# Kernel optimization log

Hardware: AMD Instinct MI355X
Metric: run time of the kernel (lower is better)

The kernel has to match this reference:

```python
import jax, jax.numpy as jnp
import numpy as np

N_NODES = 100000
N_EDGES = 1600000
IN_FEATS = 128
HEADS = 4
OUT_FEATS = 16
NEG_SLOPE = 0.2  # DGL GATConv default negative_slope


def setup_inputs() -> dict:
    key = jax.random.key(0)
    ks = jax.random.split(key, 7)
    feats = jax.random.normal(ks[0], (N_NODES, IN_FEATS), dtype=jnp.float32)
    W = jax.random.normal(ks[1], (HEADS * OUT_FEATS, IN_FEATS), dtype=jnp.float32) * 0.05
    attn_l = jax.random.normal(ks[2], (HEADS, OUT_FEATS), dtype=jnp.float32) * 0.1
    attn_r = jax.random.normal(ks[3], (HEADS, OUT_FEATS), dtype=jnp.float32) * 0.1
    bias = jax.random.normal(ks[4], (HEADS * OUT_FEATS,), dtype=jnp.float32) * 0.01
    src = jax.random.randint(ks[5], (N_EDGES,), 0, N_NODES, dtype=jnp.int64 if jax.config.jax_enable_x64 else jnp.int32)
    dst = jax.random.randint(ks[6], (N_EDGES,), 0, N_NODES, dtype=jnp.int64 if jax.config.jax_enable_x64 else jnp.int32)
    return {"feats": feats, "W": W, "attn_l": attn_l, "attn_r": attn_r,
            "bias": bias, "src": src, "dst": dst}


def reference(feats, W, attn_l, attn_r, bias, src, dst):
    """GATConv forward on a homogeneous graph built from concatenated edge lists.

    feats: [N, in_feats]; W: [H*F, in_feats]; attn_l/attn_r: [H, F]; bias: [H*F]
    src/dst: [E] edge endpoint indices. Returns [N, H, F] (DGL GATConv output).
    """
    N = feats.shape[0]
    H, F = attn_l.shape
    # Linear projection, per-head split: z [N, H, F]
    z = (feats @ W.T).reshape(N, H, F)
    # Per-node attention logits: el/er [N, H]
    el = jnp.einsum('nhf,hf->nh', z, attn_l)
    er = jnp.einsum('nhf,hf->nh', z, attn_r)
    # Per-edge unnormalized attention: e [E, H]
    e = jax.nn.leaky_relu(el[src] + er[dst], negative_slope=NEG_SLOPE)
    # Edge softmax over incoming edges of each destination node
    m = jax.ops.segment_max(e, dst, num_segments=N)           # [N, H]
    m = jnp.where(jnp.isfinite(m), m, jnp.zeros_like(m))      # guard empty segments
    ex = jnp.exp(e - m[dst])                                  # [E, H]
    denom = jax.ops.segment_sum(ex, dst, num_segments=N)      # [N, H]
    alpha = ex / denom[dst]                                   # [E, H]
    # Weighted message aggregation: scatter-add z[src] * alpha into dst
    msg = z[src] * alpha[:, :, None]                          # [E, H, F]
    out = jax.ops.segment_sum(msg, dst, num_segments=N)       # [N, H, F]
    return out + bias.reshape(1, H, F)
```

## Files before the change

kernel.cpp:

```cpp
#include <hip/hip_runtime.h>

#define N_NODES 100000
#define N_EDGES 1600000
#define IN_F    128
#define HEADS   4
#define OUT_F   16
#define HF      64
#define NEG_SLOPE 0.2f
#define NB_MFMA 1563

#define BUCK    112
#define NBUCK   893
#define BSTRIDE 2048
#define BSC_CHUNK 6144
#define NB_BSC  261
#define BUCK3   56
#define K3_BLOCKS 1786

typedef __attribute__((ext_vector_type(8))) short short8;
typedef __attribute__((ext_vector_type(4))) float f32x4;

__device__ __forceinline__ short f2bf(float f) {
    union { float f; unsigned u; } v; v.f = f;
    return (short)((v.u + 0x7FFFu + ((v.u >> 16) & 1u)) >> 16);
}

__global__ __launch_bounds__(256) void k_prep(const float* __restrict__ W,
                                              const float* __restrict__ attn_l,
                                              const float* __restrict__ attn_r,
                                              unsigned short* __restrict__ Wfrag,
                                              int* __restrict__ gcur) {
    __shared__ float Bext[16 * IN_F];
    int t = threadIdx.x;
    for (int i = t; i < NBUCK; i += 256) gcur[i] = 0;
    for (int o = t; o < 16 * IN_F; o += 256) {
        int c = o >> 7, k = o & 127;
        float v = 0.f;
        if (c < 8) {
            int hh = c & 3;
            const float* at = (c < 4) ? attn_l : attn_r;
            #pragma unroll
            for (int f = 0; f < 16; ++f)
                v += W[(size_t)(hh * 16 + f) * IN_F + k] * at[hh * 16 + f];
        }
        Bext[o] = v;
    }
    __syncthreads();
    for (int idx = t; idx < 20 * 64 * 8; idx += 256) {
        int j = idx & 7;
        int lane = (idx >> 3) & 63;
        int g = idx >> 9;
        int ct = g >> 2, kf = g & 3;
        int n = lane & 15, qq = lane >> 4;
        int k = kf * 32 + qq * 8 + j;
        float val = (ct < 4) ? W[(size_t)(ct * 16 + n) * IN_F + k]
                             : Bext[n * IN_F + k];
        Wfrag[idx] = (unsigned short)f2bf(val);
    }
}

__global__ __launch_bounds__(256) void k1_mfma(const float* __restrict__ feats,
                                               const unsigned short* __restrict__ Wfrag,
                                               unsigned short* __restrict__ zb,
                                               float* __restrict__ el,
                                               float* __restrict__ er) {
    const int t = threadIdx.x;
    const int grp = t >> 6;
    const int l = t & 63;
    const int q = l >> 4, n = l & 15;

    short8 bfrag[5][4];
    #pragma unroll
    for (int ct = 0; ct < 5; ++ct)
        #pragma unroll
        for (int kf = 0; kf < 4; ++kf)
            bfrag[ct][kf] = *(const short8*)(Wfrag + (size_t)((ct * 4 + kf) * 64 + l) * 8);

    int anode = blockIdx.x * 64 + grp * 16 + n;
    int aclamp = anode < N_NODES ? anode : 0;
    const float* arow = feats + (size_t)aclamp * IN_F + q * 8;

    f32x4 acc[5];
    #pragma unroll
    for (int ct = 0; ct < 5; ++ct) acc[ct] = (f32x4){0.f, 0.f, 0.f, 0.f};

    #pragma unroll
    for (int kf = 0; kf < 4; ++kf) {
        float4 x = *(const float4*)(arow + kf * 32);
        float4 y = *(const float4*)(arow + kf * 32 + 4);
        short8 a;
        a[0] = f2bf(x.x); a[1] = f2bf(x.y); a[2] = f2bf(x.z); a[3] = f2bf(x.w);
        a[4] = f2bf(y.x); a[5] = f2bf(y.y); a[6] = f2bf(y.z); a[7] = f2bf(y.w);
        #pragma unroll
        for (int ct = 0; ct < 5; ++ct)
            acc[ct] = __builtin_amdgcn_mfma_f32_16x16x32_bf16(a, bfrag[ct][kf], acc[ct], 0, 0, 0);
    }

    #pragma unroll
    for (int reg = 0; reg < 4; ++reg) {
        int onode = blockIdx.x * 64 + grp * 16 + q * 4 + reg;
        if (onode >= N_NODES) continue;
        #pragma unroll
        for (int ct = 0; ct < 4; ++ct)
            zb[(size_t)onode * HF + ct * 16 + n] = (unsigned short)f2bf(acc[ct][reg]);
        float v4 = acc[4][reg];
        if (n < 4)       el[onode * HEADS + n] = v4;
        else if (n < 8)  er[onode * HEADS + (n - 4)] = v4;
    }
}

__global__ __launch_bounds__(1024) void k_bsc(const int* __restrict__ src,
                                              const int* __restrict__ dst,
                                              int* __restrict__ gcur,
                                              unsigned* __restrict__ bin) {
    __shared__ int h[NBUCK], cur[NBUCK];
    const int t = threadIdx.x;
    if (t < NBUCK) { h[t] = 0; }
    __syncthreads();
    const int start = blockIdx.x * BSC_CHUNK;
    int end = start + BSC_CHUNK;
    if (end > N_EDGES) end = N_EDGES;

    int myd[6];
    #pragma unroll
    for (int k = 0; k < 6; ++k) {
        int i = start + t + k * 1024;
        myd[k] = (i < end) ? dst[i] : -1;
        if (myd[k] >= 0) atomicAdd(&h[(unsigned)myd[k] / BUCK], 1);
    }
    __syncthreads();
    if (t < NBUCK) cur[t] = h[t] ? atomicAdd(&gcur[t], h[t]) : 0;
    __syncthreads();
    #pragma unroll
    for (int k = 0; k < 6; ++k) {
        int i = start + t + k * 1024;
        if (i < end) {
            unsigned d = (unsigned)myd[k];
            unsigned b = d / BUCK;
            unsigned dl = d - b * BUCK;
            int pos = atomicAdd(&cur[b], 1);
            if (pos < BSTRIDE)
                bin[(size_t)b * BSTRIDE + pos] = (unsigned)src[i] | (dl << 17);
        }
    }
}

__global__ __launch_bounds__(256) void k3_sort(const unsigned* __restrict__ bin,
                                               const int* __restrict__ gcur,
                                               const float* __restrict__ el,
                                               const float* __restrict__ er,
                                               const unsigned short* __restrict__ zb,
                                               const float* __restrict__ bias,
                                               float* __restrict__ out) {
    __shared__ unsigned raw[BSTRIDE];
    __shared__ unsigned sorted[BSTRIDE];
    __shared__ int hist[BUCK3];
    __shared__ int noff[BUCK3 + 1];
    __shared__ int cur[BUCK3];
    __shared__ int s[64];
    __shared__ float er_s[BUCK3 * HEADS];

    const int t = threadIdx.x;
    const int B2 = blockIdx.x >> 1;
    const int half = blockIdx.x & 1;
    const int dlo = half * BUCK3;
    const int nodebase = B2 * BUCK + dlo;
    const unsigned* mybin = bin + (size_t)B2 * BSTRIDE;
    int cnt = gcur[B2];
    if (cnt > BSTRIDE) cnt = BSTRIDE;

    if (t < BUCK3) hist[t] = 0;
    if (t < BUCK3 * HEADS) {
        int g = nodebase * HEADS + t;
        er_s[t] = (g < N_NODES * HEADS) ? er[g] : 0.f;
    }
    for (int i = t; i < cnt; i += 256) raw[i] = mybin[i];
    __syncthreads();

    for (int i = t; i < cnt; i += 256) {
        int d2 = (int)(raw[i] >> 17) - dlo;
        if ((unsigned)d2 < BUCK3) atomicAdd(&hist[d2], 1);
    }
    __syncthreads();

    if (t < 64) s[t] = (t < BUCK3) ? hist[t] : 0;
    __syncthreads();
    for (int o = 1; o < 64; o <<= 1) {
        int x = (t < 64 && t >= o) ? s[t - o] : 0;
        __syncthreads();
        if (t < 64) s[t] += x;
        __syncthreads();
    }
    if (t < BUCK3) {
        int excl = s[t] - hist[t];
        noff[t] = excl;
        cur[t] = excl;
    }
    if (t == 0) noff[BUCK3] = s[BUCK3 - 1];
    __syncthreads();

    for (int i = t; i < cnt; i += 256) {
        unsigned p = raw[i];
        int d2 = (int)(p >> 17) - dlo;
        if ((unsigned)d2 < BUCK3) {
            int pos = atomicAdd(&cur[d2], 1);
            sorted[pos] = p & 0x1FFFF;
        }
    }
    __syncthreads();

    const int wave = t >> 6, lane = t & 63;
    const int j = lane >> 3;
    const int c = lane & 7;
    const int h = c >> 1;

    for (int nl = wave; nl < BUCK3; nl += 4) {
        int node = nodebase + nl;
        if (node >= N_NODES) break;
        const int nlo = noff[nl], nhi = noff[nl + 1];
        const float er_d = er_s[nl * HEADS + h];

        float4 A0 = make_float4(0.f, 0.f, 0.f, 0.f);
        float4 A1 = make_float4(0.f, 0.f, 0.f, 0.f);
        float den = 0.f;
        for (int i = nlo + j; i < nhi; i += 8) {
            int sN = sorted[i];
            float x = el[sN * HEADS + h] + er_d;
            x = x > 0.f ? x : NEG_SLOPE * x;
            float ex = __expf(x);
            den += ex;
            uint4 v = *(const uint4*)(zb + (size_t)sN * HF + c * 8);
            A0.x += ex * __uint_as_float(v.x << 16);
            A0.y += ex * __uint_as_float(v.x & 0xFFFF0000u);
            A0.z += ex * __uint_as_float(v.y << 16);
            A0.w += ex * __uint_as_float(v.y & 0xFFFF0000u);
            A1.x += ex * __uint_as_float(v.z << 16);
            A1.y += ex * __uint_as_float(v.z & 0xFFFF0000u);
            A1.z += ex * __uint_as_float(v.w << 16);
            A1.w += ex * __uint_as_float(v.w & 0xFFFF0000u);
        }
        #pragma unroll
        for (int m = 8; m <= 32; m <<= 1) {
            A0.x += __shfl_xor(A0.x, m); A0.y += __shfl_xor(A0.y, m);
            A0.z += __shfl_xor(A0.z, m); A0.w += __shfl_xor(A0.w, m);
            A1.x += __shfl_xor(A1.x, m); A1.y += __shfl_xor(A1.y, m);
            A1.z += __shfl_xor(A1.z, m); A1.w += __shfl_xor(A1.w, m);
            den  += __shfl_xor(den,  m);
        }
        if (j == 0) {
            float4 b0 = *(const float4*)(bias + c * 8);
            float4 b1 = *(const float4*)(bias + c * 8 + 4);
            if (den > 0.f) {
                float inv = 1.f / den;
                b0.x += A0.x * inv; b0.y += A0.y * inv;
                b0.z += A0.z * inv; b0.w += A0.w * inv;
                b1.x += A1.x * inv; b1.y += A1.y * inv;
                b1.z += A1.z * inv; b1.w += A1.w * inv;
            }
            *(float4*)(out + (size_t)node * HF + c * 8) = b0;
            *(float4*)(out + (size_t)node * HF + c * 8 + 4) = b1;
        }
    }
}

extern "C" void kernel_launch(void* const* d_in, const int* in_sizes, int n_in,
                              void* d_out, int out_size, void* d_ws, size_t ws_size,
                              hipStream_t stream) {
    const float* feats  = (const float*)d_in[0];
    const float* W      = (const float*)d_in[1];
    const float* attn_l = (const float*)d_in[2];
    const float* attn_r = (const float*)d_in[3];
    const float* bias   = (const float*)d_in[4];
    const int*   src    = (const int*)d_in[5];
    const int*   dst    = (const int*)d_in[6];
    float* out = (float*)d_out;

    char* ws = (char*)d_ws;
    unsigned short* zb = (unsigned short*)ws;  ws += (size_t)N_NODES * HF * 2;
    float* el    = (float*)ws;                 ws += N_NODES * HEADS * 4;
    float* er    = (float*)ws;                 ws += N_NODES * HEADS * 4;
    unsigned short* Wfrag = (unsigned short*)ws; ws += 20 * 64 * 8 * 2;
    int*   gcur  = (int*)ws;                   ws += 1024 * 4;
    unsigned* bin = (unsigned*)ws;             ws += (size_t)NBUCK * BSTRIDE * 4;

    k_prep  <<<1,         256,  0, stream>>>(W, attn_l, attn_r, Wfrag, gcur);
    k1_mfma <<<NB_MFMA,   256,  0, stream>>>(feats, Wfrag, zb, el, er);
    k_bsc   <<<NB_BSC,    1024, 0, stream>>>(src, dst, gcur, bin);
    k3_sort <<<K3_BLOCKS, 256,  0, stream>>>(bin, gcur, el, er, zb, bias, out);
}
```

Before: 189.5 us.

## Use coarser dst buckets with ballot compaction in sort-aggregate kernel

Replaces the 893 fine destination buckets with 224 coarse buckets of 448 nodes, so the binning pass runs fewer global atomics and writes less scattered output. Each k3 block now takes a 112-node sub-range, uses 512 threads, and compacts its matching edges from the coarse bin into shared memory with wave ballot and popcount before the histogram and sort. Each block now reads the whole coarse bin (about four times the data it needs), which trades extra read traffic for cheaper scattering. The MFMA kernel also switches to packed bf16 conversion intrinsics.

```diff
diff --git a/kernel.cpp b/kernel.cpp
--- a/kernel.cpp
+++ b/kernel.cpp
@@ -1,4 +1,5 @@
 #include <hip/hip_runtime.h>
+#include <hip/hip_bf16.h>
 
 #define N_NODES 100000
 #define N_EDGES 1600000
@@ -9,13 +10,15 @@
 #define NEG_SLOPE 0.2f
 #define NB_MFMA 1563
 
-#define BUCK    112
-#define NBUCK   893
-#define BSTRIDE 2048
+#define CBUCK   448
+#define NCB     224
+#define CSTRIDE 7936
 #define BSC_CHUNK 6144
 #define NB_BSC  261
-#define BUCK3   56
-#define K3_BLOCKS 1786
+
+#define SUB     112
+#define K3_BLOCKS 896
+#define RAWCAP  2304
 
 typedef __attribute__((ext_vector_type(8))) short short8;
 typedef __attribute__((ext_vector_type(4))) float f32x4;
@@ -23,6 +26,12 @@
 __device__ __forceinline__ short f2bf(float f) {
     union { float f; unsigned u; } v; v.f = f;
     return (short)((v.u + 0x7FFFu + ((v.u >> 16) & 1u)) >> 16);
+}
+
+__device__ __forceinline__ unsigned pkbf(float a, float b) {
+    __hip_bfloat162 t = __float22bfloat162_rn(make_float2(a, b));
+    unsigned r; __builtin_memcpy(&r, &t, sizeof(r));
+    return r;
 }
 
 __global__ __launch_bounds__(256) void k_prep(const float* __restrict__ W,
@@ -32,7 +41,7 @@
                                               int* __restrict__ gcur) {
     __shared__ float Bext[16 * IN_F];
     int t = threadIdx.x;
-    for (int i = t; i < NBUCK; i += 256) gcur[i] = 0;
+    for (int i = t; i < 1024; i += 256) gcur[i] = 0;
     for (int o = t; o < 16 * IN_F; o += 256) {
         int c = o >> 7, k = o & 127;
         float v = 0.f;
@@ -89,8 +98,11 @@
         float4 x = *(const float4*)(arow + kf * 32);
         float4 y = *(const float4*)(arow + kf * 32 + 4);
         short8 a;
-        a[0] = f2bf(x.x); a[1] = f2bf(x.y); a[2] = f2bf(x.z); a[3] = f2bf(x.w);
-        a[4] = f2bf(y.x); a[5] = f2bf(y.y); a[6] = f2bf(y.z); a[7] = f2bf(y.w);
+        unsigned* au = (unsigned*)&a;
+        au[0] = pkbf(x.x, x.y);
+        au[1] = pkbf(x.z, x.w);
+        au[2] = pkbf(y.x, y.y);
+        au[3] = pkbf(y.z, y.w);
         #pragma unroll
         for (int ct = 0; ct < 5; ++ct)
             acc[ct] = __builtin_amdgcn_mfma_f32_16x16x32_bf16(a, bfrag[ct][kf], acc[ct], 0, 0, 0);
@@ -113,9 +125,9 @@
                                               const int* __restrict__ dst,
                                               int* __restrict__ gcur,
                                               unsigned* __restrict__ bin) {
-    __shared__ int h[NBUCK], cur[NBUCK];
+    __shared__ int h[NCB], cur[NCB];
     const int t = threadIdx.x;
-    if (t < NBUCK) { h[t] = 0; }
+    if (t < NCB) h[t] = 0;
     __syncthreads();
     const int start = blockIdx.x * BSC_CHUNK;
     int end = start + BSC_CHUNK;
@@ -126,95 +138,109 @@
     for (int k = 0; k < 6; ++k) {
         int i = start + t + k * 1024;
         myd[k] = (i < end) ? dst[i] : -1;
-        if (myd[k] >= 0) atomicAdd(&h[(unsigned)myd[k] / BUCK], 1);
-    }
-    __syncthreads();
-    if (t < NBUCK) cur[t] = h[t] ? atomicAdd(&gcur[t], h[t]) : 0;
+        if (myd[k] >= 0) atomicAdd(&h[(unsigned)myd[k] / CBUCK], 1);
+    }
+    __syncthreads();
+    if (t < NCB) cur[t] = h[t] ? atomicAdd(&gcur[t], h[t]) : 0;
     __syncthreads();
     #pragma unroll
     for (int k = 0; k < 6; ++k) {
         int i = start + t + k * 1024;
         if (i < end) {
             unsigned d = (unsigned)myd[k];
-            unsigned b = d / BUCK;
-            unsigned dl = d - b * BUCK;
+            unsigned b = d / CBUCK;
+            unsigned dl = d - b * CBUCK;
             int pos = atomicAdd(&cur[b], 1);
-            if (pos < BSTRIDE)
-                bin[(size_t)b * BSTRIDE + pos] = (unsigned)src[i] | (dl << 17);
-        }
-    }
-}
-
-__global__ __launch_bounds__(256) void k3_sort(const unsigned* __restrict__ bin,
+            if (pos < CSTRIDE)
+                bin[(size_t)b * CSTRIDE + pos] = (unsigned)src[i] | (dl << 17);
+        }
+    }
+}
+
+__global__ __launch_bounds__(512) void k3_sort(const unsigned* __restrict__ bin,
                                                const int* __restrict__ gcur,
                                                const float* __restrict__ el,
                                                const float* __restrict__ er,
                                                const unsigned short* __restrict__ zb,
                                                const float* __restrict__ bias,
                                                float* __restrict__ out) {
-    __shared__ unsigned raw[BSTRIDE];
-    __shared__ unsigned sorted[BSTRIDE];
-    __shared__ int hist[BUCK3];
-    __shared__ int noff[BUCK3 + 1];
-    __shared__ int cur[BUCK3];
-    __shared__ int s[64];
-    __shared__ float er_s[BUCK3 * HEADS];
+    __shared__ unsigned raw[RAWCAP];
+    __shared__ unsigned sorted[RAWCAP];
+    __shared__ int hist[SUB];
+    __shared__ int noff[SUB + 1];
+    __shared__ int cur[SUB];
+    __shared__ int s[128];
+    __shared__ float er_s[SUB * HEADS];
+    __shared__ int rawcnt;
 
     const int t = threadIdx.x;
-    const int B2 = blockIdx.x >> 1;
-    const int half = blockIdx.x & 1;
-    const int dlo = half * BUCK3;
-    const int nodebase = B2 * BUCK + dlo;
-    const unsigned* mybin = bin + (size_t)B2 * BSTRIDE;
-    int cnt = gcur[B2];
-    if (cnt > BSTRIDE) cnt = BSTRIDE;
-
-    if (t < BUCK3) hist[t] = 0;
-    if (t < BUCK3 * HEADS) {
+    const int B = blockIdx.x >> 2;
+    const int sub = blockIdx.x & 3;
+    const int dlo = sub * SUB;
+    const int nodebase = B * CBUCK + dlo;
+    const unsigned* mybin = bin + (size_t)B * CSTRIDE;
+    int cnt = gcur[B];
+    if (cnt > CSTRIDE) cnt = CSTRIDE;
+
+    if (t < SUB) hist[t] = 0;
+    if (t == 0) rawcnt = 0;
+    if (t < SUB * HEADS) {
         int g = nodebase * HEADS + t;
         er_s[t] = (g < N_NODES * HEADS) ? er[g] : 0.f;
     }
-    for (int i = t; i < cnt; i += 256) raw[i] = mybin[i];
-    __syncthreads();
-
-    for (int i = t; i < cnt; i += 256) {
-        int d2 = (int)(raw[i] >> 17) - dlo;
-        if ((unsigned)d2 < BUCK3) atomicAdd(&hist[d2], 1);
-    }
-    __syncthreads();
-
-    if (t < 64) s[t] = (t < BUCK3) ? hist[t] : 0;
-    __syncthreads();
-    for (int o = 1; o < 64; o <<= 1) {
-        int x = (t < 64 && t >= o) ? s[t - o] : 0;
+    __syncthreads();
+
+    const int lane = t & 63;
+    for (int i0 = 0; i0 < cnt; i0 += 512) {
+        int e = i0 + t;
+        bool valid = e < cnt;
+        unsigned p = valid ? mybin[e] : 0u;
+        int d2 = (int)(p >> 17) - dlo;
+        bool match = valid && ((unsigned)d2 < (unsigned)SUB);
+        unsigned long long mask = __ballot(match);
+        int wbase = 0;
+        if (lane == 0) wbase = atomicAdd(&rawcnt, __popcll(mask));
+        wbase = __shfl(wbase, 0, 64);
+        int pos = wbase + __popcll(mask & ((1ull << lane) - 1ull));
+        if (match && pos < RAWCAP)
+            raw[pos] = (p & 0x1FFFFu) | ((unsigned)d2 << 17);
+    }
+    __syncthreads();
+    int rn = rawcnt < RAWCAP ? rawcnt : RAWCAP;
+
+    for (int i = t; i < rn; i += 512)
+        atomicAdd(&hist[raw[i] >> 17], 1);
+    __syncthreads();
+
+    if (t < 128) s[t] = (t < SUB) ? hist[t] : 0;
+    __syncthreads();
+    for (int o = 1; o < 128; o <<= 1) {
+        int x = (t < 128 && t >= o) ? s[t - o] : 0;
         __syncthreads();
-        if (t < 64) s[t] += x;
+        if (t < 128) s[t] += x;
         __syncthreads();
     }
-    if (t < BUCK3) {
+    if (t < SUB) {
         int excl = s[t] - hist[t];
         noff[t] = excl;
         cur[t] = excl;
     }
-    if (t == 0) noff[BUCK3] = s[BUCK3 - 1];
-    __syncthreads();
-
-    for (int i = t; i < cnt; i += 256) {
+    if (t == 0) noff[SUB] = s[SUB - 1];
+    __syncthreads();
+
+    for (int i = t; i < rn; i += 512) {
         unsigned p = raw[i];
-        int d2 = (int)(p >> 17) - dlo;
-        if ((unsigned)d2 < BUCK3) {
-            int pos = atomicAdd(&cur[d2], 1);
-            sorted[pos] = p & 0x1FFFF;
-        }
-    }
-    __syncthreads();
-
-    const int wave = t >> 6, lane = t & 63;
+        int pos = atomicAdd(&cur[p >> 17], 1);
+        sorted[pos] = p & 0x1FFFFu;
+    }
+    __syncthreads();
+
+    const int wave = t >> 6;
     const int j = lane >> 3;
     const int c = lane & 7;
     const int h = c >> 1;
 
-    for (int nl = wave; nl < BUCK3; nl += 4) {
+    for (int nl = wave; nl < SUB; nl += 8) {
         int node = nodebase + nl;
         if (node >= N_NODES) break;
         const int nlo = noff[nl], nhi = noff[nl + 1];
@@ -281,10 +307,10 @@
     float* er    = (float*)ws;                 ws += N_NODES * HEADS * 4;
     unsigned short* Wfrag = (unsigned short*)ws; ws += 20 * 64 * 8 * 2;
     int*   gcur  = (int*)ws;                   ws += 1024 * 4;
-    unsigned* bin = (unsigned*)ws;             ws += (size_t)NBUCK * BSTRIDE * 4;
+    unsigned* bin = (unsigned*)ws;             ws += (size_t)NCB * CSTRIDE * 4;
 
     k_prep  <<<1,         256,  0, stream>>>(W, attn_l, attn_r, Wfrag, gcur);
     k1_mfma <<<NB_MFMA,   256,  0, stream>>>(feats, Wfrag, zb, el, er);
     k_bsc   <<<NB_BSC,    1024, 0, stream>>>(src, dst, gcur, bin);
-    k3_sort <<<K3_BLOCKS, 256,  0, stream>>>(bin, gcur, el, er, zb, bias, out);
-}
+    k3_sort <<<K3_BLOCKS, 512,  0, stream>>>(bin, gcur, el, er, zb, bias, out);
+}
```

New measurement: 192.9 us. No clear change (+1.8%).
